# Kernel optimization log

Hardware: AMD Instinct MI355X
Metric: run time of the kernel (lower is better)

Reference implementation:

```python
import jax, jax.numpy as jnp
import numpy as np

B, T, P, D, S, R = 4, 128, 256, 512, 64, 8  # batch, window, patches, d_model, n_state, dt_rank


def setup_inputs() -> dict:
    key = jax.random.key(0)
    ks = jax.random.split(key, 8)
    sc = 0.02  # weight init scale
    return {
        "X": jax.random.normal(ks[0], (B, T, P, D), jnp.float32),
        "H0": jnp.zeros((B, P, S), jnp.float32),
        "a_hat": jax.random.normal(ks[1], (S,), jnp.float32),
        "U_w": jax.random.normal(ks[2], (S, D), jnp.float32) * sc,
        "sB_w": jax.random.normal(ks[3], (S, D), jnp.float32) * sc,
        "sB_b": jnp.zeros((S,), jnp.float32),
        "sC_w": jax.random.normal(ks[4], (S, D), jnp.float32) * sc,
        "sC_b": jnp.zeros((S,), jnp.float32),
        "sD1_w": jax.random.normal(ks[5], (R, D), jnp.float32) * sc,
        "sD1_b": jnp.zeros((R,), jnp.float32),
        "sD2_w": jax.random.normal(ks[6], (1, R), jnp.float32) * sc,
        "sD2_b": jnp.zeros((1,), jnp.float32),
        "ro_w": jax.random.normal(ks[7], (D, S), jnp.float32) * sc,
    }


def reference(X, H0, a_hat, U_w, sB_w, sB_b, sC_w, sC_b, sD1_w, sD1_b, sD2_w, sD2_b, ro_w):
    eps = 1e-12
    logA = -jnp.exp(a_hat)                                    # [S]
    # selective (input-dependent) parameters
    u = jnp.einsum('btpd,sd->btps', X, U_w)                   # [B,T,P,S]
    B_t = jnp.einsum('btpd,sd->btps', X, sB_w) + sB_b
    C_t = jnp.einsum('btpd,sd->btps', X, sC_w) + sC_b
    dt_feat = jax.nn.silu(jnp.einsum('btpd,rd->btpr', X, sD1_w) + sD1_b)
    dt = jax.nn.softplus(jnp.einsum('btpr,or->btpo', dt_feat, sD2_w) + sD2_b)  # [B,T,P,1]
    A = jnp.exp(dt * logA)                                    # [B,T,P,S] via broadcast
    b = (1.0 - A) * (B_t * u)
    # prefix-product scan: h_t = A_t*h_{t-1} + b_t  ->  h_t = P_t*(H0 + cumsum(b/P))
    Pc = jnp.cumprod(jnp.maximum(A, eps), axis=1)             # [B,T,P,S]
    invP = 1.0 / jnp.maximum(Pc, eps)
    c = jnp.cumsum(b * invP, axis=1)
    H_seq = Pc * (H0[:, None] + c)                            # [B,T,P,S]
    Y_seq = jnp.einsum('btps,ds->btpd', C_t * H_seq, ro_w)    # [B,T,P,D]
    Y_seq = Y_seq.reshape(X.shape[0], -1, X.shape[-1])        # [B, T*P, D]
    H_T = H_seq[:, -1]                                        # [B,P,S]
    return (H_seq, Y_seq, H_T)
```

## Files before the change

### kernel.cpp

```cpp
#include <hip/hip_runtime.h>
#include <hip/hip_bf16.h>
#include <math.h>

namespace {
constexpr int B_N = 4, T_N = 128, P_N = 256, D_N = 512, S_N = 64;
constexpr int NTH = 512;
constexpr int KC  = 32;
constexpr int NCH = D_N / KC;

constexpr int XS0_OFF = 0;
constexpr int WS0_OFF = 8192;
constexpr int XS1_OFF = 24576;
constexpr int WS1_OFF = 32768;
constexpr int BU_OFF  = 0;
constexpr int CH_OFF  = 16384;
constexpr int HS_OFF  = 32768;
constexpr int ROS0_OFF= 0;
constexpr int ROS1_OFF= 16384;
constexpr int DT_OFF  = 65536;
constexpr int LDS_BYTES = 66048;

constexpr int WIMG_ELEMS  = NCH * 256 * 32;
constexpr int ROIMG_ELEMS = 4 * 128 * 64;
}

typedef short bf16x8 __attribute__((ext_vector_type(8)));
typedef float f32x4  __attribute__((ext_vector_type(4)));

__device__ __forceinline__ unsigned short f2b(float f) {
    unsigned int x = __float_as_uint(f);
    return (unsigned short)((x + 0x7FFFu + ((x >> 16) & 1u)) >> 16);
}
__device__ __forceinline__ float b2f(unsigned short h) {
    return __uint_as_float(((unsigned int)h) << 16);
}
__device__ __forceinline__ unsigned int pk2(float lo, float hi) {
    union { __hip_bfloat162 h; unsigned int u; } cv;
    cv.h = __float22bfloat162_rn(float2{lo, hi});
    return cv.u;
}
__device__ __forceinline__ int swz32(int row, int col) {
    return row * 32 + (col ^ (((row >> 1) & 3) << 3));
}
__device__ __forceinline__ int swz64(int row, int col) {
    return row * 64 + (col ^ ((row & 7) << 3));
}
__device__ __forceinline__ void cvtstore8(unsigned short* dst, float4 a, float4 b) {
    uint4 r;
    r.x = pk2(a.x, a.y); r.y = pk2(a.z, a.w);
    r.z = pk2(b.x, b.y); r.w = pk2(b.z, b.w);
    *(uint4*)dst = r;
}
__device__ __forceinline__ void gload16(const void* g, void* l) {
    __builtin_amdgcn_global_load_lds(
        (const __attribute__((address_space(1))) unsigned int*)g,
        (__attribute__((address_space(3))) unsigned int*)l, 16, 0, 0);
}

__global__ __launch_bounds__(512) void mamba_prep(
    const float* __restrict__ U_w, const float* __restrict__ sB_w,
    const float* __restrict__ sC_w, const float* __restrict__ sD1_w,
    const float* __restrict__ ro_w,
    unsigned short* __restrict__ wImg, unsigned short* __restrict__ roImg)
{
    const int idx = blockIdx.x * 512 + threadIdx.x;
    if (idx < WIMG_ELEMS) {
        const int kc = idx >> 13, rem = idx & 8191, r = rem >> 5, c = rem & 31;
        float v = 0.0f;
        if (r < 192) {
            const int g = r >> 4, w = r & 15, tr = g % 3, sb = g / 3;
            const float* base = (tr == 0) ? U_w : (tr == 1) ? sB_w : sC_w;
            v = base[(size_t)(sb * 16 + w) * D_N + kc * KC + c];
        } else if (r < 200) {
            v = sD1_w[(size_t)(r - 192) * D_N + kc * KC + c];
        }
        wImg[kc * 8192 + swz32(r, c)] = f2b(v);
    } else if (idx < WIMG_ELEMS + ROIMG_ELEMS) {
        const int j = idx - WIMG_ELEMS;
        const int pp = j >> 13, rem = j & 8191, r = rem >> 6, c = rem & 63;
        roImg[pp * 8192 + swz64(r, c)] = f2b(ro_w[(size_t)(pp * 128 + r) * S_N + c]);
    }
}

__global__ __launch_bounds__(NTH, 4) void mamba_mfma(
    const float* __restrict__ X, const float* __restrict__ H0,
    const float* __restrict__ a_hat,
    const float* __restrict__ sB_b, const float* __restrict__ sC_b,
    const float* __restrict__ sD1_b, const float* __restrict__ sD2_w,
    const float* __restrict__ sD2_b,
    const unsigned short* __restrict__ wImg, const unsigned short* __restrict__ roImg,
    float* __restrict__ Hseq, float* __restrict__ Y, float* __restrict__ HT)
{
    __shared__ __align__(16) char smem[LDS_BYTES];
    float* DTB = (float*)(smem + DT_OFF);

    const int tid  = threadIdx.x;
    const int lane = tid & 63;
    const int wid  = tid >> 6;
    const int wm   = wid >> 2;
    const int wn   = wid & 3;
    const int l15  = lane & 15;
    const int lg   = lane >> 4;
    const int lane16 = lane * 16;
    const int b    = blockIdx.x >> 8;
    const int p    = blockIdx.x & 255;
    const char* wImgB  = (const char*)wImg;
    const char* roImgB = (const char*)roImg;

    const float la  = (tid < 64) ? -expf(a_hat[tid]) : 0.0f;
    const float h0v = (tid < 64) ? H0[((size_t)b * P_N + p) * S_N + tid] : 0.0f;

    f32x4 acc[4][3];
    f32x4 accdt;
    #pragma unroll
    for (int q = 0; q < 4; ++q) accdt[q] = 0.0f;
    #pragma unroll
    for (int mf = 0; mf < 4; ++mf)
        #pragma unroll
        for (int nf = 0; nf < 3; ++nf)
            #pragma unroll
            for (int q = 0; q < 4; ++q) acc[mf][nf][q] = 0.0f;

    const int xr = tid >> 2, xq = tid & 3;
    const float* xsrc = X + (((size_t)b * T_N + xr) * P_N + p) * D_N + xq * 8;
    const int xoff = swz32(xr, xq * 8);

    float4 xA, xB;
    {
        float4 t0 = *(const float4*)(xsrc), t1 = *(const float4*)(xsrc + 4);
        cvtstore8((unsigned short*)(smem + XS0_OFF) + xoff, t0, t1);
        gload16(wImgB + wid * 2048 + lane16,        smem + WS0_OFF + wid * 2048);
        gload16(wImgB + wid * 2048 + 1024 + lane16, smem + WS0_OFF + wid * 2048 + 1024);
        const float* n1 = xsrc + KC;
        xA = *(const float4*)(n1); xB = *(const float4*)(n1 + 4);
    }
    __syncthreads();

    const int kb = lg * 8;
    #pragma unroll 2
    for (int kc = 0; kc < NCH; ++kc) {
        unsigned short* XSc = (unsigned short*)(smem + ((kc & 1) ? XS1_OFF : XS0_OFF));
        unsigned short* WSc = (unsigned short*)(smem + ((kc & 1) ? WS1_OFF : WS0_OFF));
        char*           XSn = smem + ((kc & 1) ? XS0_OFF : XS1_OFF);
        char*           WSn = smem + ((kc & 1) ? WS0_OFF : WS1_OFF);
        if (kc + 1 < NCH) {
            cvtstore8((unsigned short*)XSn + xoff, xA, xB);
            gload16(wImgB + (kc + 1) * 16384 + wid * 2048 + lane16,        WSn + wid * 2048);
            gload16(wImgB + (kc + 1) * 16384 + wid * 2048 + 1024 + lane16, WSn + wid * 2048 + 1024);
        }
        if (kc + 2 < NCH) {
            const float* nx = xsrc + (kc + 2) * KC;
            xA = *(const float4*)(nx); xB = *(const float4*)(nx + 4);
        }
        __builtin_amdgcn_s_setprio(1);
        bf16x8 a[4];
        #pragma unroll
        for (int mf = 0; mf < 4; ++mf)
            a[mf] = *(const bf16x8*)&XSc[swz32(wm * 64 + mf * 16 + l15, kb)];
        #pragma unroll
        for (int nf = 0; nf < 3; ++nf) {
            bf16x8 bb = *(const bf16x8*)&WSc[swz32(wn * 48 + nf * 16 + l15, kb)];
            #pragma unroll
            for (int mf = 0; mf < 4; ++mf)
                acc[mf][nf] = __builtin_amdgcn_mfma_f32_16x16x32_bf16(a[mf], bb, acc[mf][nf], 0, 0, 0);
        }
        {
            bf16x8 adt = *(const bf16x8*)&XSc[swz32(wid * 16 + l15, kb)];
            bf16x8 bd  = *(const bf16x8*)&WSc[swz32(192 + l15, kb)];
            accdt = __builtin_amdgcn_mfma_f32_16x16x32_bf16(adt, bd, accdt, 0, 0, 0);
        }
        __builtin_amdgcn_s_setprio(0);
        __syncthreads();
    }

    {
        unsigned short* BU  = (unsigned short*)(smem + BU_OFF);
        unsigned short* CHB = (unsigned short*)(smem + CH_OFF);
        const int s = wn * 16 + l15;
        const float biasB = sB_b[s], biasC = sC_b[s];
        #pragma unroll
        for (int mf = 0; mf < 4; ++mf) {
            #pragma unroll
            for (int q = 0; q < 4; ++q) {
                const int t = wm * 64 + mf * 16 + lg * 4 + q;
                const float u  = acc[mf][0][q];
                const float Bv = acc[mf][1][q] + biasB;
                const float Cv = acc[mf][2][q] + biasC;
                BU[t * 64 + s]   = f2b(Bv * u);
                CHB[swz64(t, s)] = f2b(Cv);
            }
        }
    }
    {
        const float w2 = (l15 < 8) ? sD2_w[l15] : 0.0f;
        const float b1 = (l15 < 8) ? sD1_b[l15] : 0.0f;
        const float b2 = sD2_b[0];
        #pragma unroll
        for (int q = 0; q < 4; ++q) {
            float z = accdt[q] + b1;
            float w = (z / (1.0f + expf(-z))) * w2;
            w = (l15 < 8) ? w : 0.0f;
            w += __shfl_xor(w, 1);
            w += __shfl_xor(w, 2);
            w += __shfl_xor(w, 4);
            if (l15 == 0) {
                float zz = w + b2;
                DTB[wid * 16 + lg * 4 + q] = (zz > 20.0f) ? zz : log1pf(expf(zz));
            }
        }
    }
    __syncthreads();

    if (tid < 64) {
        unsigned short* BU   = (unsigned short*)(smem + BU_OFF);
        float*          HSEQ = (float*)(smem + HS_OFF);
        const int s = tid;
        float Pcv = 1.0f, cv = 0.0f, Hv = 0.0f;
        float bn[4], dn[4];
        #pragma unroll
        for (int q = 0; q < 4; ++q) { bn[q] = b2f(BU[q * 64 + s]); dn[q] = DTB[q]; }
        for (int t0 = 0; t0 < T_N; t0 += 4) {
            float bc[4], dc[4];
            #pragma unroll
            for (int q = 0; q < 4; ++q) { bc[q] = bn[q]; dc[q] = dn[q]; }
            if (t0 + 4 < T_N) {
                #pragma unroll
                for (int q = 0; q < 4; ++q) {
                    bn[q] = b2f(BU[(t0 + 4 + q) * 64 + s]);
                    dn[q] = DTB[t0 + 4 + q];
                }
            }
            #pragma unroll
            for (int q = 0; q < 4; ++q) {
                const float Av = expf(dc[q] * la);
                const float bv = (1.0f - Av) * bc[q];
                Pcv *= fmaxf(Av, 1e-12f);
                cv += bv * (1.0f / fmaxf(Pcv, 1e-12f));
                Hv = Pcv * (h0v + cv);
                HSEQ[(t0 + q) * 64 + s] = Hv;
            }
        }
        HT[((size_t)b * P_N + p) * S_N + s] = Hv;
    }
    __syncthreads();

    gload16(roImgB + wid * 2048 + lane16,        smem + ROS0_OFF + wid * 2048);
    gload16(roImgB + wid * 2048 + 1024 + lane16, smem + ROS0_OFF + wid * 2048 + 1024);
    {
        float*          HSEQ = (float*)(smem + HS_OFF);
        unsigned short* CHB  = (unsigned short*)(smem + CH_OFF);
        const int r  = tid >> 2;
        const int c0 = (((tid & 3) + r) & 3) * 16;
        float4 h0 = *(const float4*)&HSEQ[r * 64 + c0];
        float4 h1 = *(const float4*)&HSEQ[r * 64 + c0 + 4];
        float4 h2 = *(const float4*)&HSEQ[r * 64 + c0 + 8];
        float4 h3 = *(const float4*)&HSEQ[r * 64 + c0 + 12];
        float* hout = Hseq + (((size_t)b * T_N + r) * P_N + p) * S_N + c0;
        *(float4*)(hout)      = h0;
        *(float4*)(hout + 4)  = h1;
        *(float4*)(hout + 8)  = h2;
        *(float4*)(hout + 12) = h3;
        bf16x8 ca = *(const bf16x8*)&CHB[swz64(r, c0)];
        bf16x8 cb = *(const bf16x8*)&CHB[swz64(r, c0 + 8)];
        bf16x8 oa, ob;
        oa[0] = (short)f2b(b2f((unsigned short)ca[0]) * h0.x);
        oa[1] = (short)f2b(b2f((unsigned short)ca[1]) * h0.y);
        oa[2] = (short)f2b(b2f((unsigned short)ca[2]) * h0.z);
        oa[3] = (short)f2b(b2f((unsigned short)ca[3]) * h0.w);
        oa[4] = (short)f2b(b2f((unsigned short)ca[4]) * h1.x);
        oa[5] = (short)f2b(b2f((unsigned short)ca[5]) * h1.y);
        oa[6] = (short)f2b(b2f((unsigned short)ca[6]) * h1.z);
        oa[7] = (short)f2b(b2f((unsigned short)ca[7]) * h1.w);
        ob[0] = (short)f2b(b2f((unsigned short)cb[0]) * h2.x);
        ob[1] = (short)f2b(b2f((unsigned short)cb[1]) * h2.y);
        ob[2] = (short)f2b(b2f((unsigned short)cb[2]) * h2.z);
        ob[3] = (short)f2b(b2f((unsigned short)cb[3]) * h2.w);
        ob[4] = (short)f2b(b2f((unsigned short)cb[4]) * h3.x);
        ob[5] = (short)f2b(b2f((unsigned short)cb[5]) * h3.y);
        ob[6] = (short)f2b(b2f((unsigned short)cb[6]) * h3.z);
        ob[7] = (short)f2b(b2f((unsigned short)cb[7]) * h3.w);
        *(bf16x8*)&CHB[swz64(r, c0)]     = oa;
        *(bf16x8*)&CHB[swz64(r, c0 + 8)] = ob;
    }
    __syncthreads();

    bf16x8 af0[4], af1[4];
    {
        unsigned short* CHB = (unsigned short*)(smem + CH_OFF);
        #pragma unroll
        for (int mf = 0; mf < 4; ++mf) {
            af0[mf] = *(const bf16x8*)&CHB[swz64(wm * 64 + mf * 16 + l15, lg * 8)];
            af1[mf] = *(const bf16x8*)&CHB[swz64(wm * 64 + mf * 16 + l15, 32 + lg * 8)];
        }
    }
    __syncthreads();

    for (int pp = 0; pp < 4; ++pp) {
        unsigned short* cur = (unsigned short*)(smem + ((pp & 1) ? ROS1_OFF : ROS0_OFF));
        char*           nxt = smem + ((pp & 1) ? ROS0_OFF : ROS1_OFF);
        if (pp < 3) {
            gload16(roImgB + (pp + 1) * 16384 + wid * 2048 + lane16,        nxt + wid * 2048);
            gload16(roImgB + (pp + 1) * 16384 + wid * 2048 + 1024 + lane16, nxt + wid * 2048 + 1024);
        }
        f32x4 yacc[4][2];
        #pragma unroll
        for (int mf = 0; mf < 4; ++mf)
            #pragma unroll
            for (int nf = 0; nf < 2; ++nf)
                #pragma unroll
                for (int q = 0; q < 4; ++q) yacc[mf][nf][q] = 0.0f;
        #pragma unroll
        for (int nf = 0; nf < 2; ++nf) {
            bf16x8 bb0 = *(const bf16x8*)&cur[swz64(wn * 32 + nf * 16 + l15, lg * 8)];
            bf16x8 bb1 = *(const bf16x8*)&cur[swz64(wn * 32 + nf * 16 + l15, 32 + lg * 8)];
            #pragma unroll
            for (int mf = 0; mf < 4; ++mf) {
                yacc[mf][nf] = __builtin_amdgcn_mfma_f32_16x16x32_bf16(bb0, af0[mf], yacc[mf][nf], 0, 0, 0);
                yacc[mf][nf] = __builtin_amdgcn_mfma_f32_16x16x32_bf16(bb1, af1[mf], yacc[mf][nf], 0, 0, 0);
            }
        }
        #pragma unroll
        for (int mf = 0; mf < 4; ++mf) {
            const int t = wm * 64 + mf * 16 + l15;
            float* ybase = Y + (((size_t)b * T_N + t) * P_N + p) * D_N;
            #pragma unroll
            for (int nf = 0; nf < 2; ++nf) {
                const int d = pp * 128 + wn * 32 + nf * 16 + lg * 4;
                *(float4*)(ybase + d) = make_float4(yacc[mf][nf][0], yacc[mf][nf][1],
                                                    yacc[mf][nf][2], yacc[mf][nf][3]);
            }
        }
        if (pp < 3) __syncthreads();
    }
}

extern "C" void kernel_launch(void* const* d_in, const int* in_sizes, int n_in,
                              void* d_out, int out_size, void* d_ws, size_t ws_size,
                              hipStream_t stream) {
    const float* X     = (const float*)d_in[0];
    const float* H0    = (const float*)d_in[1];
    const float* a_hat = (const float*)d_in[2];
    const float* U_w   = (const float*)d_in[3];
    const float* sB_w  = (const float*)d_in[4];
    const float* sB_b  = (const float*)d_in[5];
    const float* sC_w  = (const float*)d_in[6];
    const float* sC_b  = (const float*)d_in[7];
    const float* sD1_w = (const float*)d_in[8];
    const float* sD1_b = (const float*)d_in[9];
    const float* sD2_w = (const float*)d_in[10];
    const float* sD2_b = (const float*)d_in[11];
    const float* ro_w  = (const float*)d_in[12];

    float* out   = (float*)d_out;
    float* HseqP = out;
    float* YP    = out + (size_t)B_N * T_N * P_N * S_N;
    float* HTP   = YP  + (size_t)B_N * T_N * P_N * D_N;

    unsigned short* wImg  = (unsigned short*)d_ws;
    unsigned short* roImg = (unsigned short*)((char*)d_ws + 262144);

    hipLaunchKernelGGL(mamba_prep, dim3((WIMG_ELEMS + ROIMG_ELEMS) / 512), dim3(512), 0, stream,
                       U_w, sB_w, sC_w, sD1_w, ro_w, wImg, roImg);
    hipLaunchKernelGGL(mamba_mfma, dim3(B_N * P_N), dim3(NTH), 0, stream,
                       X, H0, a_hat, sB_b, sC_b, sD1_b, sD2_w, sD2_b,
                       wImg, roImg, HseqP, YP, HTP);
}
```

Baseline: 153.0 us.

## Read weight fragments directly from global memory and double K chunk size

Weight and readout operands are no longer staged into LDS through global_load_lds. Each wave now loads its MFMA B fragments straight from row-major bf16 images in global memory, relying on the cache. The X chunk width grows from 32 to 64, which halves the number of K iterations and barriers, and the readout loop drops its per-stage syncs. In exchange, every wave issues many small uncoalesced global loads inside the MFMA loop, adding latency that LDS staging used to hide.

```diff
diff --git a/kernel.cpp b/kernel.cpp
--- a/kernel.cpp
+++ b/kernel.cpp
@@ -5,23 +5,20 @@
 namespace {
 constexpr int B_N = 4, T_N = 128, P_N = 256, D_N = 512, S_N = 64;
 constexpr int NTH = 512;
-constexpr int KC  = 32;
+constexpr int KC  = 64;
 constexpr int NCH = D_N / KC;
 
 constexpr int XS0_OFF = 0;
-constexpr int WS0_OFF = 8192;
-constexpr int XS1_OFF = 24576;
-constexpr int WS1_OFF = 32768;
-constexpr int BU_OFF  = 0;
-constexpr int CH_OFF  = 16384;
-constexpr int HS_OFF  = 32768;
-constexpr int ROS0_OFF= 0;
-constexpr int ROS1_OFF= 16384;
+constexpr int XS1_OFF = 16384;
+constexpr int BU_OFF  = 32768;
+constexpr int CH_OFF  = 49152;
+constexpr int HS_OFF  = 0;
 constexpr int DT_OFF  = 65536;
 constexpr int LDS_BYTES = 66048;
 
-constexpr int WIMG_ELEMS  = NCH * 256 * 32;
-constexpr int ROIMG_ELEMS = 4 * 128 * 64;
+constexpr int W2_ROWS  = 208;
+constexpr int W2_ELEMS = W2_ROWS * D_N;
+constexpr int RO2_ELEMS = D_N * S_N;
 }
 
 typedef short bf16x8 __attribute__((ext_vector_type(8)));
@@ -38,9 +35,6 @@
     union { __hip_bfloat162 h; unsigned int u; } cv;
     cv.h = __float22bfloat162_rn(float2{lo, hi});
     return cv.u;
-}
-__device__ __forceinline__ int swz32(int row, int col) {
-    return row * 32 + (col ^ (((row >> 1) & 3) << 3));
 }
 __device__ __forceinline__ int swz64(int row, int col) {
     return row * 64 + (col ^ ((row & 7) << 3));
@@ -50,11 +44,6 @@
     r.x = pk2(a.x, a.y); r.y = pk2(a.z, a.w);
     r.z = pk2(b.x, b.y); r.w = pk2(b.z, b.w);
     *(uint4*)dst = r;
-}
-__device__ __forceinline__ void gload16(const void* g, void* l) {
-    __builtin_amdgcn_global_load_lds(
-        (const __attribute__((address_space(1))) unsigned int*)g,
-        (__attribute__((address_space(3))) unsigned int*)l, 16, 0, 0);
 }
 
 __global__ __launch_bounds__(512) void mamba_prep(
@@ -64,21 +53,20 @@
     unsigned short* __restrict__ wImg, unsigned short* __restrict__ roImg)
 {
     const int idx = blockIdx.x * 512 + threadIdx.x;
-    if (idx < WIMG_ELEMS) {
-        const int kc = idx >> 13, rem = idx & 8191, r = rem >> 5, c = rem & 31;
+    if (idx < W2_ELEMS) {
+        const int r = idx >> 9, c = idx & 511;
         float v = 0.0f;
         if (r < 192) {
             const int g = r >> 4, w = r & 15, tr = g % 3, sb = g / 3;
             const float* base = (tr == 0) ? U_w : (tr == 1) ? sB_w : sC_w;
-            v = base[(size_t)(sb * 16 + w) * D_N + kc * KC + c];
+            v = base[(size_t)(sb * 16 + w) * D_N + c];
         } else if (r < 200) {
-            v = sD1_w[(size_t)(r - 192) * D_N + kc * KC + c];
-        }
-        wImg[kc * 8192 + swz32(r, c)] = f2b(v);
-    } else if (idx < WIMG_ELEMS + ROIMG_ELEMS) {
-        const int j = idx - WIMG_ELEMS;
-        const int pp = j >> 13, rem = j & 8191, r = rem >> 6, c = rem & 63;
-        roImg[pp * 8192 + swz64(r, c)] = f2b(ro_w[(size_t)(pp * 128 + r) * S_N + c]);
+            v = sD1_w[(size_t)(r - 192) * D_N + c];
+        }
+        wImg[idx] = f2b(v);
+    } else if (idx < W2_ELEMS + RO2_ELEMS) {
+        const int j = idx - W2_ELEMS;
+        roImg[j] = f2b(ro_w[j]);
     }
 }
 
@@ -101,11 +89,8 @@
     const int wn   = wid & 3;
     const int l15  = lane & 15;
     const int lg   = lane >> 4;
-    const int lane16 = lane * 16;
     const int b    = blockIdx.x >> 8;
     const int p    = blockIdx.x & 255;
-    const char* wImgB  = (const char*)wImg;
-    const char* roImgB = (const char*)roImg;
 
     const float la  = (tid < 64) ? -expf(a_hat[tid]) : 0.0f;
     const float h0v = (tid < 64) ? H0[((size_t)b * P_N + p) * S_N + tid] : 0.0f;
@@ -122,52 +107,55 @@
             for (int q = 0; q < 4; ++q) acc[mf][nf][q] = 0.0f;
 
     const int xr = tid >> 2, xq = tid & 3;
-    const float* xsrc = X + (((size_t)b * T_N + xr) * P_N + p) * D_N + xq * 8;
-    const int xoff = swz32(xr, xq * 8);
-
-    float4 xA, xB;
-    {
-        float4 t0 = *(const float4*)(xsrc), t1 = *(const float4*)(xsrc + 4);
-        cvtstore8((unsigned short*)(smem + XS0_OFF) + xoff, t0, t1);
-        gload16(wImgB + wid * 2048 + lane16,        smem + WS0_OFF + wid * 2048);
-        gload16(wImgB + wid * 2048 + 1024 + lane16, smem + WS0_OFF + wid * 2048 + 1024);
+    const float* xsrc = X + (((size_t)b * T_N + xr) * P_N + p) * D_N + xq * 16;
+    const int xo0 = swz64(xr, xq * 16);
+    const int xo1 = swz64(xr, xq * 16 + 8);
+
+    float4 xA, xB, xC, xD;
+    {
+        float4 t0 = *(const float4*)(xsrc),     t1 = *(const float4*)(xsrc + 4);
+        float4 t2 = *(const float4*)(xsrc + 8), t3 = *(const float4*)(xsrc + 12);
+        cvtstore8((unsigned short*)(smem + XS0_OFF) + xo0, t0, t1);
+        cvtstore8((unsigned short*)(smem + XS0_OFF) + xo1, t2, t3);
         const float* n1 = xsrc + KC;
-        xA = *(const float4*)(n1); xB = *(const float4*)(n1 + 4);
+        xA = *(const float4*)(n1);     xB = *(const float4*)(n1 + 4);
+        xC = *(const float4*)(n1 + 8); xD = *(const float4*)(n1 + 12);
     }
     __syncthreads();
 
-    const int kb = lg * 8;
     #pragma unroll 2
     for (int kc = 0; kc < NCH; ++kc) {
         unsigned short* XSc = (unsigned short*)(smem + ((kc & 1) ? XS1_OFF : XS0_OFF));
-        unsigned short* WSc = (unsigned short*)(smem + ((kc & 1) ? WS1_OFF : WS0_OFF));
-        char*           XSn = smem + ((kc & 1) ? XS0_OFF : XS1_OFF);
-        char*           WSn = smem + ((kc & 1) ? WS0_OFF : WS1_OFF);
+        unsigned short* XSn = (unsigned short*)(smem + ((kc & 1) ? XS0_OFF : XS1_OFF));
         if (kc + 1 < NCH) {
-            cvtstore8((unsigned short*)XSn + xoff, xA, xB);
-            gload16(wImgB + (kc + 1) * 16384 + wid * 2048 + lane16,        WSn + wid * 2048);
-            gload16(wImgB + (kc + 1) * 16384 + wid * 2048 + 1024 + lane16, WSn + wid * 2048 + 1024);
+            cvtstore8(XSn + xo0, xA, xB);
+            cvtstore8(XSn + xo1, xC, xD);
         }
         if (kc + 2 < NCH) {
             const float* nx = xsrc + (kc + 2) * KC;
-            xA = *(const float4*)(nx); xB = *(const float4*)(nx + 4);
+            xA = *(const float4*)(nx);     xB = *(const float4*)(nx + 4);
+            xC = *(const float4*)(nx + 8); xD = *(const float4*)(nx + 12);
         }
         __builtin_amdgcn_s_setprio(1);
-        bf16x8 a[4];
-        #pragma unroll
-        for (int mf = 0; mf < 4; ++mf)
-            a[mf] = *(const bf16x8*)&XSc[swz32(wm * 64 + mf * 16 + l15, kb)];
-        #pragma unroll
-        for (int nf = 0; nf < 3; ++nf) {
-            bf16x8 bb = *(const bf16x8*)&WSc[swz32(wn * 48 + nf * 16 + l15, kb)];
+        #pragma unroll
+        for (int kf = 0; kf < 2; ++kf) {
+            const int kb = kf * 32 + lg * 8;
+            bf16x8 a[4];
             #pragma unroll
             for (int mf = 0; mf < 4; ++mf)
-                acc[mf][nf] = __builtin_amdgcn_mfma_f32_16x16x32_bf16(a[mf], bb, acc[mf][nf], 0, 0, 0);
-        }
-        {
-            bf16x8 adt = *(const bf16x8*)&XSc[swz32(wid * 16 + l15, kb)];
-            bf16x8 bd  = *(const bf16x8*)&WSc[swz32(192 + l15, kb)];
-            accdt = __builtin_amdgcn_mfma_f32_16x16x32_bf16(adt, bd, accdt, 0, 0, 0);
+                a[mf] = *(const bf16x8*)&XSc[swz64(wm * 64 + mf * 16 + l15, kb)];
+            #pragma unroll
+            for (int nf = 0; nf < 3; ++nf) {
+                bf16x8 bb = *(const bf16x8*)(wImg + (size_t)(wn * 48 + nf * 16 + l15) * D_N + kc * KC + kb);
+                #pragma unroll
+                for (int mf = 0; mf < 4; ++mf)
+                    acc[mf][nf] = __builtin_amdgcn_mfma_f32_16x16x32_bf16(a[mf], bb, acc[mf][nf], 0, 0, 0);
+            }
+            {
+                bf16x8 adt = *(const bf16x8*)&XSc[swz64(wid * 16 + l15, kb)];
+                bf16x8 bd  = *(const bf16x8*)(wImg + (size_t)(192 + l15) * D_N + kc * KC + kb);
+                accdt = __builtin_amdgcn_mfma_f32_16x16x32_bf16(adt, bd, accdt, 0, 0, 0);
+            }
         }
         __builtin_amdgcn_s_setprio(0);
         __syncthreads();
@@ -244,8 +232,6 @@
     }
     __syncthreads();
 
-    gload16(roImgB + wid * 2048 + lane16,        smem + ROS0_OFF + wid * 2048);
-    gload16(roImgB + wid * 2048 + 1024 + lane16, smem + ROS0_OFF + wid * 2048 + 1024);
     {
         float*          HSEQ = (float*)(smem + HS_OFF);
         unsigned short* CHB  = (unsigned short*)(smem + CH_OFF);
@@ -293,15 +279,8 @@
             af1[mf] = *(const bf16x8*)&CHB[swz64(wm * 64 + mf * 16 + l15, 32 + lg * 8)];
         }
     }
-    __syncthreads();
 
     for (int pp = 0; pp < 4; ++pp) {
-        unsigned short* cur = (unsigned short*)(smem + ((pp & 1) ? ROS1_OFF : ROS0_OFF));
-        char*           nxt = smem + ((pp & 1) ? ROS0_OFF : ROS1_OFF);
-        if (pp < 3) {
-            gload16(roImgB + (pp + 1) * 16384 + wid * 2048 + lane16,        nxt + wid * 2048);
-            gload16(roImgB + (pp + 1) * 16384 + wid * 2048 + 1024 + lane16, nxt + wid * 2048 + 1024);
-        }
         f32x4 yacc[4][2];
         #pragma unroll
         for (int mf = 0; mf < 4; ++mf)
@@ -311,8 +290,9 @@
                 for (int q = 0; q < 4; ++q) yacc[mf][nf][q] = 0.0f;
         #pragma unroll
         for (int nf = 0; nf < 2; ++nf) {
-            bf16x8 bb0 = *(const bf16x8*)&cur[swz64(wn * 32 + nf * 16 + l15, lg * 8)];
-            bf16x8 bb1 = *(const bf16x8*)&cur[swz64(wn * 32 + nf * 16 + l15, 32 + lg * 8)];
+            const unsigned short* rp = roImg + (size_t)(pp * 128 + wn * 32 + nf * 16 + l15) * S_N;
+            bf16x8 bb0 = *(const bf16x8*)(rp + lg * 8);
+            bf16x8 bb1 = *(const bf16x8*)(rp + 32 + lg * 8);
             #pragma unroll
             for (int mf = 0; mf < 4; ++mf) {
                 yacc[mf][nf] = __builtin_amdgcn_mfma_f32_16x16x32_bf16(bb0, af0[mf], yacc[mf][nf], 0, 0, 0);
@@ -330,7 +310,6 @@
                                                     yacc[mf][nf][2], yacc[mf][nf][3]);
             }
         }
-        if (pp < 3) __syncthreads();
     }
 }
 
@@ -357,9 +336,9 @@
     float* HTP   = YP  + (size_t)B_N * T_N * P_N * D_N;
 
     unsigned short* wImg  = (unsigned short*)d_ws;
-    unsigned short* roImg = (unsigned short*)((char*)d_ws + 262144);
-
-    hipLaunchKernelGGL(mamba_prep, dim3((WIMG_ELEMS + ROIMG_ELEMS) / 512), dim3(512), 0, stream,
+    unsigned short* roImg = (unsigned short*)((char*)d_ws + W2_ELEMS * 2);
+
+    hipLaunchKernelGGL(mamba_prep, dim3((W2_ELEMS + RO2_ELEMS) / 512), dim3(512), 0, stream,
                        U_w, sB_w, sC_w, sD1_w, ro_w, wImg, roImg);
     hipLaunchKernelGGL(mamba_mfma, dim3(B_N * P_N), dim3(NTH), 0, stream,
                        X, H0, a_hat, sB_b, sC_b, sD1_b, sD2_w, sD2_b,
```

Measured after the change: 259.1 us. +69.4%, slower.
